# Optimization experiments

Measured on AMD Instinct MI355X. Metric: run time of the kernel, lower is better.

Reference implementation:

```python
import jax, jax.numpy as jnp
import numpy as np

N = 65536        # nodes
E = 1048576      # edges (avg degree 16)
IN, HID, OUT = 128, 64, 64


def setup_inputs() -> dict:
    key = jax.random.key(0)
    ks = jax.random.split(key, 6)
    x = jax.random.normal(ks[0], (N, IN), jnp.float32)
    edge_index = jax.random.randint(ks[1], (2, E), 0, N, jnp.int32)
    # Glorot-style init as in PyG GCNConv
    W1 = jax.random.normal(ks[2], (IN, HID), jnp.float32) * (1.0 / np.sqrt(IN))
    b1 = jnp.zeros((HID,), jnp.float32)
    W2 = jax.random.normal(ks[3], (HID, OUT), jnp.float32) * (1.0 / np.sqrt(HID))
    b2 = jnp.zeros((OUT,), jnp.float32)
    return {"x": x, "edge_index": edge_index, "W1": W1, "b1": b1, "W2": W2, "b2": b2}


def _gcn_conv(h, src, dst, dinv_sqrt, W, b):
    # PyG GCNConv: transform, then D^-1/2 A_hat D^-1/2 aggregation (A_hat has self-loops)
    h = h @ W                                   # [N, F_out]
    norm = dinv_sqrt[src] * dinv_sqrt[dst]      # [E+N]
    msg = h[src] * norm[:, None]                # gather + scale
    return jax.ops.segment_sum(msg, dst, num_segments=N) + b


def reference(x, edge_index, W1, b1, W2, b2):
    loops = jnp.arange(N, dtype=edge_index.dtype)
    src = jnp.concatenate([edge_index[0], loops])   # [E+N] with self-loops
    dst = jnp.concatenate([edge_index[1], loops])
    deg = jax.ops.segment_sum(jnp.ones_like(dst, x.dtype), dst, num_segments=N)
    dinv_sqrt = jax.lax.rsqrt(deg)                  # deg >= 1 thanks to self-loops
    h = jax.nn.relu(_gcn_conv(x, src, dst, dinv_sqrt, W1, b1))
    return _gcn_conv(h, src, dst, dinv_sqrt, W2, b2)
```

## Files before the change

### kernel.cpp

```cpp
#include <hip/hip_runtime.h>
#include <hip/hip_fp16.h>


#define N_NODES 65536
#define E_EDGES 1048576
#define F_IN    128
#define F_HID   64
#define CAPSH   6
#define GEMM1_BLOCKS (N_NODES / 64)
#define FILL_BLOCKS  ((E_EDGES / 4 / 256) * 8)

__device__ inline unsigned int pack_h2(float a, float b) {
    __half2 h = __floats2half2_rn(a, b);
    return *(unsigned int*)&h;
}

__device__ inline float4 h4_to_f4(uint2 q) {
    __half2 a = *(__half2*)&q.x;
    __half2 b = *(__half2*)&q.y;
    float2 fa = __half22float2(a), fb = __half22float2(b);
    return make_float4(fa.x, fa.y, fb.x, fb.y);
}

template <int F_K, bool SCALED>
__device__ inline void gemm_body(const float* __restrict__ h, const float* __restrict__ W,
                                 const int* __restrict__ cnt, __half* __restrict__ P,
                                 int bid) {
    int wave = __builtin_amdgcn_readfirstlane(threadIdx.x >> 6);
    int lane = threadIdx.x & 63;
    int v = bid * 64 + lane;
    const float4* hr = (const float4*)(h + (size_t)v * F_K);
    float4 acc[4];
#pragma unroll
    for (int j = 0; j < 4; ++j) acc[j] = make_float4(0.f, 0.f, 0.f, 0.f);
#pragma unroll 4
    for (int kb = 0; kb < F_K / 4; ++kb) {
        float4 hv = hr[kb];
#pragma unroll
        for (int r = 0; r < 4; ++r) {
            float hk = r == 0 ? hv.x : r == 1 ? hv.y : r == 2 ? hv.z : hv.w;
            const float4* Wr = (const float4*)(W + (size_t)(kb * 4 + r) * 64 + (wave << 4));
#pragma unroll
            for (int j = 0; j < 4; ++j) {
                float4 w = Wr[j];
                acc[j].x = fmaf(hk, w.x, acc[j].x);
                acc[j].y = fmaf(hk, w.y, acc[j].y);
                acc[j].z = fmaf(hk, w.z, acc[j].z);
                acc[j].w = fmaf(hk, w.w, acc[j].w);
            }
        }
    }
    float s = SCALED ? rsqrtf((float)cnt[v] + 1.0f) : 1.0f;
    __half* Pr = P + (size_t)v * 64 + (wave << 4);
    uint4 q0, q1;
    q0.x = pack_h2(acc[0].x * s, acc[0].y * s); q0.y = pack_h2(acc[0].z * s, acc[0].w * s);
    q0.z = pack_h2(acc[1].x * s, acc[1].y * s); q0.w = pack_h2(acc[1].z * s, acc[1].w * s);
    q1.x = pack_h2(acc[2].x * s, acc[2].y * s); q1.y = pack_h2(acc[2].z * s, acc[2].w * s);
    q1.z = pack_h2(acc[3].x * s, acc[3].y * s); q1.w = pack_h2(acc[3].z * s, acc[3].w * s);
    ((uint4*)Pr)[0] = q0;
    ((uint4*)Pr)[1] = q1;
}

__global__ __launch_bounds__(256) void k_fused(
        const float* __restrict__ x, const float* __restrict__ W1,
        __half* __restrict__ P,
        const int* __restrict__ src, const int* __restrict__ dst,
        int* __restrict__ cnt, unsigned short* __restrict__ csr) {
    if (blockIdx.x < GEMM1_BLOCKS) {
        gemm_body<F_IN, false>(x, W1, nullptr, P, blockIdx.x);
    } else {
        int fb    = blockIdx.x - GEMM1_BLOCKS;
        int g     = fb & 7;
        int chunk = fb >> 3;
        int i     = chunk * blockDim.x + threadIdx.x;
        int4 d = ((const int4*)dst)[i];
#pragma unroll
        for (int k = 0; k < 4; ++k) {
            int dv = k == 0 ? d.x : k == 1 ? d.y : k == 2 ? d.z : d.w;
            if ((dv >> 13) == g) {
                int pos = atomicAdd(&cnt[dv], 1);
                csr[(dv << CAPSH) + pos] = (unsigned short)src[4 * i + k];
            }
        }
    }
}

__global__ __launch_bounds__(256) void k_scale(
        __half* __restrict__ P, const int* __restrict__ cnt) {
    int t = blockIdx.x * blockDim.x + threadIdx.x;
    int v = t >> 2;
    float dv = rsqrtf((float)cnt[v] + 1.0f);
    uint4* p = (uint4*)(P + (size_t)v * 64) + (t & 3) * 2;
#pragma unroll
    for (int q = 0; q < 2; ++q) {
        uint4 u = p[q];
        unsigned int* w = (unsigned int*)&u;
#pragma unroll
        for (int j = 0; j < 4; ++j) {
            __half2 h = *(__half2*)&w[j];
            float2 f = __half22float2(h);
            w[j] = pack_h2(f.x * dv, f.y * dv);
        }
        p[q] = u;
    }
}

template <int F_K>
__global__ __launch_bounds__(256) void k_gemm(
        const float* __restrict__ h, const float* __restrict__ W,
        const int* __restrict__ cnt, __half* __restrict__ P) {
    gemm_body<F_K, true>(h, W, cnt, P, blockIdx.x);
}

template <bool RELU>
__global__ __launch_bounds__(256) void k_agg(
        const __half* __restrict__ P, const unsigned short* __restrict__ csr,
        const int* __restrict__ cnt, const float* __restrict__ b,
        float* __restrict__ out) {
    int lane = threadIdx.x & 63;
    int sub  = lane >> 4;
    int col4 = lane & 15;
    int wave  = (blockIdx.x * blockDim.x + threadIdx.x) >> 6;
    int nwave = (gridDim.x * blockDim.x) >> 6;
    float4 bias = ((const float4*)b)[col4];
    for (int v = wave; v < N_NODES; v += nwave) {
        int c    = cnt[v];
        float dv = rsqrtf((float)c + 1.0f);
        int sidx = csr[(v << CAPSH) + lane];
        float4 acc = make_float4(0.f, 0.f, 0.f, 0.f);
        if (sub == 0) {
            float4 p = h4_to_f4(((const uint2*)(P + (size_t)v * 64))[col4]);
            acc = p;
        }
        for (int i = 0; i < c; i += 16) {
#pragma unroll
            for (int u = 0; u < 4; ++u) {
                int e = i + sub + 4 * u;
                int s = __shfl(sidx, e);
                if (e < c) {
                    float4 p = h4_to_f4(((const uint2*)(P + (size_t)s * 64))[col4]);
                    acc.x += p.x; acc.y += p.y; acc.z += p.z; acc.w += p.w;
                }
            }
        }
        acc.x += __shfl_xor(acc.x, 16); acc.y += __shfl_xor(acc.y, 16);
        acc.z += __shfl_xor(acc.z, 16); acc.w += __shfl_xor(acc.w, 16);
        acc.x += __shfl_xor(acc.x, 32); acc.y += __shfl_xor(acc.y, 32);
        acc.z += __shfl_xor(acc.z, 32); acc.w += __shfl_xor(acc.w, 32);
        if (lane < 16) {
            float4 o;
            o.x = dv * acc.x + bias.x;
            o.y = dv * acc.y + bias.y;
            o.z = dv * acc.z + bias.z;
            o.w = dv * acc.w + bias.w;
            if (RELU) {
                o.x = o.x > 0.f ? o.x : 0.f;
                o.y = o.y > 0.f ? o.y : 0.f;
                o.z = o.z > 0.f ? o.z : 0.f;
                o.w = o.w > 0.f ? o.w : 0.f;
            }
            ((float4*)(out + (size_t)v * 64))[col4] = o;
        }
    }
}

extern "C" void kernel_launch(void* const* d_in, const int* in_sizes, int n_in,
                              void* d_out, int out_size, void* d_ws, size_t ws_size,
                              hipStream_t stream) {
    const float* x   = (const float*)d_in[0];
    const int*   ei  = (const int*)d_in[1];
    const float* W1  = (const float*)d_in[2];
    const float* b1  = (const float*)d_in[3];
    const float* W2  = (const float*)d_in[4];
    const float* b2  = (const float*)d_in[5];
    float*       out = (float*)d_out;

    const int* src = ei;
    const int* dst = ei + E_EDGES;

    int*            cnt = (int*)d_ws;
    unsigned short* csr = (unsigned short*)(cnt + N_NODES);
    __half*         P1  = (__half*)(csr + ((size_t)N_NODES << CAPSH));
    __half*         P2  = P1 + (size_t)N_NODES * 64;
    float*          H   = out;

    hipMemsetAsync(cnt, 0, N_NODES * sizeof(int), stream);

    k_fused<<<GEMM1_BLOCKS + FILL_BLOCKS, 256, 0, stream>>>(x, W1, P1, src, dst, cnt, csr);

    k_scale<<<N_NODES * 4 / 256, 256, 0, stream>>>(P1, cnt);

    k_agg<true><<<4096, 256, 0, stream>>>(P1, csr, cnt, b1, H);

    k_gemm<F_HID><<<N_NODES / 64, 256, 0, stream>>>(H, W2, cnt, P2);
    k_agg<false><<<4096, 256, 0, stream>>>(P2, csr, cnt, b2, out);
}
```

Before: 208.4 us.

## Interleave GEMM and CSR-fill blocks; prefetch next node and predicate gathers in aggregation

The fused kernel now interleaves GEMM1 blocks with CSR-fill blocks, 8 GEMM per 64 fill blocks. The aim is to mix compute-bound and atomic/memory-bound work across the GPU instead of running them in two phases. The aggregation kernel software-pipelines the per-node metadata by loading count, neighbour indices and the self row for the next node before processing the current one. It also issues gather loads unconditionally and masks them to zero, avoiding divergent branches. The masked loads read slot entries past the count, which may contain stale indices. These are still valid addresses because they are 16-bit indices into P, so they add extra memory traffic but stay safe.

```diff
diff --git a/kernel.cpp b/kernel.cpp
--- a/kernel.cpp
+++ b/kernel.cpp
@@ -7,8 +7,7 @@
 #define F_IN    128
 #define F_HID   64
 #define CAPSH   6
-#define GEMM1_BLOCKS (N_NODES / 64)
-#define FILL_BLOCKS  ((E_EDGES / 4 / 256) * 8)
+#define FUSED_BLOCKS 9216
 
 __device__ inline unsigned int pack_h2(float a, float b) {
     __half2 h = __floats2half2_rn(a, b);
@@ -66,12 +65,13 @@
         __half* __restrict__ P,
         const int* __restrict__ src, const int* __restrict__ dst,
         int* __restrict__ cnt, unsigned short* __restrict__ csr) {
-    if (blockIdx.x < GEMM1_BLOCKS) {
-        gemm_body<F_IN, false>(x, W1, nullptr, P, blockIdx.x);
+    int w = blockIdx.x / 72;
+    int r = blockIdx.x - w * 72;
+    if (r >= 64) {
+        gemm_body<F_IN, false>(x, W1, nullptr, cnt ? P : P, w * 8 + (r - 64));
     } else {
-        int fb    = blockIdx.x - GEMM1_BLOCKS;
-        int g     = fb & 7;
-        int chunk = fb >> 3;
+        int g     = r & 7;
+        int chunk = w * 8 + (r >> 3);
         int i     = chunk * blockDim.x + threadIdx.x;
         int4 d = ((const int4*)dst)[i];
 #pragma unroll
@@ -123,24 +123,37 @@
     int wave  = (blockIdx.x * blockDim.x + threadIdx.x) >> 6;
     int nwave = (gridDim.x * blockDim.x) >> 6;
     float4 bias = ((const float4*)b)[col4];
-    for (int v = wave; v < N_NODES; v += nwave) {
-        int c    = cnt[v];
+    int v = wave;
+    int c = 0, sidx = 0;
+    uint2 selfq = make_uint2(0u, 0u);
+    if (v < N_NODES) {
+        c     = cnt[v];
+        sidx  = csr[(v << CAPSH) + lane];
+        selfq = ((const uint2*)(P + (size_t)v * 64))[col4];
+    }
+    while (v < N_NODES) {
+        int vn = v + nwave;
+        int cn = 0, sidxn = 0;
+        uint2 selfqn = make_uint2(0u, 0u);
+        if (vn < N_NODES) {
+            cn     = cnt[vn];
+            sidxn  = csr[(vn << CAPSH) + lane];
+            selfqn = ((const uint2*)(P + (size_t)vn * 64))[col4];
+        }
         float dv = rsqrtf((float)c + 1.0f);
-        int sidx = csr[(v << CAPSH) + lane];
         float4 acc = make_float4(0.f, 0.f, 0.f, 0.f);
-        if (sub == 0) {
-            float4 p = h4_to_f4(((const uint2*)(P + (size_t)v * 64))[col4]);
-            acc = p;
-        }
+        if (sub == 0) acc = h4_to_f4(selfq);
         for (int i = 0; i < c; i += 16) {
 #pragma unroll
             for (int u = 0; u < 4; ++u) {
                 int e = i + sub + 4 * u;
                 int s = __shfl(sidx, e);
-                if (e < c) {
-                    float4 p = h4_to_f4(((const uint2*)(P + (size_t)s * 64))[col4]);
-                    acc.x += p.x; acc.y += p.y; acc.z += p.z; acc.w += p.w;
-                }
+                uint2 q = ((const uint2*)(P + (size_t)s * 64))[col4];
+                bool m = e < c;
+                q.x = m ? q.x : 0u;
+                q.y = m ? q.y : 0u;
+                float4 p = h4_to_f4(q);
+                acc.x += p.x; acc.y += p.y; acc.z += p.z; acc.w += p.w;
             }
         }
         acc.x += __shfl_xor(acc.x, 16); acc.y += __shfl_xor(acc.y, 16);
@@ -161,6 +174,7 @@
             }
             ((float4*)(out + (size_t)v * 64))[col4] = o;
         }
+        v = vn; c = cn; sidx = sidxn; selfq = selfqn;
     }
 }
 
@@ -186,7 +200,7 @@
 
     hipMemsetAsync(cnt, 0, N_NODES * sizeof(int), stream);
 
-    k_fused<<<GEMM1_BLOCKS + FILL_BLOCKS, 256, 0, stream>>>(x, W1, P1, src, dst, cnt, csr);
+    k_fused<<<FUSED_BLOCKS, 256, 0, stream>>>(x, W1, P1, src, dst, cnt, csr);
 
     k_scale<<<N_NODES * 4 / 256, 256, 0, stream>>>(P1, cnt);
 
```

Result: faster. 199.8 us (-4.1%).

## Interleave four nodes per wave in aggregation to raise memory-level parallelism

Applied to the files above, without the earlier changes.

Each wave in the aggregation kernel now processes four nodes at a time instead of looping over one node at a time. All index, count and self-row loads for the four nodes are issued up front, and gathers for all four are issued before any accumulation, so more memory requests are in flight per wave. The final store is spread so each 16-lane group writes a different node. This uses more registers, which may lower occupancy, and the wave loops up to the largest degree of its four nodes. It also hardcodes the grid of 4096 blocks to cover exactly N nodes.

```diff
diff --git a/kernel.cpp b/kernel.cpp
--- a/kernel.cpp
+++ b/kernel.cpp
@@ -112,6 +112,35 @@
     gemm_body<F_K, true>(h, W, cnt, P, blockIdx.x);
 }
 
+#define GATHER4(qq, sidx, cc)                                              \
+    if (i < cc) {                                                          \
+        _Pragma("unroll")                                                  \
+        for (int u = 0; u < 4; ++u) {                                      \
+            int e = i + sub + 4 * u;                                       \
+            int s = __shfl(sidx, e);                                       \
+            qq[u] = ((const uint2*)(P + (size_t)s * 64))[col4];            \
+        }                                                                  \
+    }
+
+#define ACC4(accv, qq, cc)                                                 \
+    if (i < cc) {                                                          \
+        _Pragma("unroll")                                                  \
+        for (int u = 0; u < 4; ++u) {                                      \
+            int e = i + sub + 4 * u;                                       \
+            bool m = e < cc;                                               \
+            uint2 q = qq[u];                                               \
+            q.x = m ? q.x : 0u; q.y = m ? q.y : 0u;                        \
+            float4 p = h4_to_f4(q);                                        \
+            accv.x += p.x; accv.y += p.y; accv.z += p.z; accv.w += p.w;    \
+        }                                                                  \
+    }
+
+#define FOLD(accv)                                                         \
+    accv.x += __shfl_xor(accv.x, 16); accv.y += __shfl_xor(accv.y, 16);    \
+    accv.z += __shfl_xor(accv.z, 16); accv.w += __shfl_xor(accv.w, 16);    \
+    accv.x += __shfl_xor(accv.x, 32); accv.y += __shfl_xor(accv.y, 32);    \
+    accv.z += __shfl_xor(accv.z, 32); accv.w += __shfl_xor(accv.w, 32);
+
 template <bool RELU>
 __global__ __launch_bounds__(256) void k_agg(
         const __half* __restrict__ P, const unsigned short* __restrict__ csr,
@@ -120,48 +149,47 @@
     int lane = threadIdx.x & 63;
     int sub  = lane >> 4;
     int col4 = lane & 15;
-    int wave  = (blockIdx.x * blockDim.x + threadIdx.x) >> 6;
-    int nwave = (gridDim.x * blockDim.x) >> 6;
+    int wid  = (blockIdx.x * blockDim.x + threadIdx.x) >> 6;
+    const int W = 16384;
+    int vA = wid, vB = wid + W, vC = wid + 2 * W, vD = wid + 3 * W;
+    int cA = cnt[vA], cB = cnt[vB], cC = cnt[vC], cD = cnt[vD];
+    int sA = csr[(vA << CAPSH) + lane], sB = csr[(vB << CAPSH) + lane];
+    int sC = csr[(vC << CAPSH) + lane], sD = csr[(vD << CAPSH) + lane];
+    uint2 qsA = ((const uint2*)(P + (size_t)vA * 64))[col4];
+    uint2 qsB = ((const uint2*)(P + (size_t)vB * 64))[col4];
+    uint2 qsC = ((const uint2*)(P + (size_t)vC * 64))[col4];
+    uint2 qsD = ((const uint2*)(P + (size_t)vD * 64))[col4];
+    float4 accA = make_float4(0.f, 0.f, 0.f, 0.f), accB = accA, accC = accA, accD = accA;
+    if (sub == 0) {
+        accA = h4_to_f4(qsA); accB = h4_to_f4(qsB);
+        accC = h4_to_f4(qsC); accD = h4_to_f4(qsD);
+    }
+    int cm = max(max(cA, cB), max(cC, cD));
+    for (int i = 0; i < cm; i += 16) {
+        uint2 qa[4], qb[4], qc[4], qd[4];
+        GATHER4(qa, sA, cA) GATHER4(qb, sB, cB)
+        GATHER4(qc, sC, cC) GATHER4(qd, sD, cD)
+        ACC4(accA, qa, cA) ACC4(accB, qb, cB)
+        ACC4(accC, qc, cC) ACC4(accD, qd, cD)
+    }
+    FOLD(accA) FOLD(accB) FOLD(accC) FOLD(accD)
+    int   vs = sub == 0 ? vA : sub == 1 ? vB : sub == 2 ? vC : vD;
+    int   cs = sub == 0 ? cA : sub == 1 ? cB : sub == 2 ? cC : cD;
+    float4 a = sub == 0 ? accA : sub == 1 ? accB : sub == 2 ? accC : accD;
+    float dv = rsqrtf((float)cs + 1.0f);
     float4 bias = ((const float4*)b)[col4];
-    for (int v = wave; v < N_NODES; v += nwave) {
-        int c    = cnt[v];
-        float dv = rsqrtf((float)c + 1.0f);
-        int sidx = csr[(v << CAPSH) + lane];
-        float4 acc = make_float4(0.f, 0.f, 0.f, 0.f);
-        if (sub == 0) {
-            float4 p = h4_to_f4(((const uint2*)(P + (size_t)v * 64))[col4]);
-            acc = p;
-        }
-        for (int i = 0; i < c; i += 16) {
-#pragma unroll
-            for (int u = 0; u < 4; ++u) {
-                int e = i + sub + 4 * u;
-                int s = __shfl(sidx, e);
-                if (e < c) {
-                    float4 p = h4_to_f4(((const uint2*)(P + (size_t)s * 64))[col4]);
-                    acc.x += p.x; acc.y += p.y; acc.z += p.z; acc.w += p.w;
-                }
-            }
-        }
-        acc.x += __shfl_xor(acc.x, 16); acc.y += __shfl_xor(acc.y, 16);
-        acc.z += __shfl_xor(acc.z, 16); acc.w += __shfl_xor(acc.w, 16);
-        acc.x += __shfl_xor(acc.x, 32); acc.y += __shfl_xor(acc.y, 32);
-        acc.z += __shfl_xor(acc.z, 32); acc.w += __shfl_xor(acc.w, 32);
-        if (lane < 16) {
-            float4 o;
-            o.x = dv * acc.x + bias.x;
-            o.y = dv * acc.y + bias.y;
-            o.z = dv * acc.z + bias.z;
-            o.w = dv * acc.w + bias.w;
-            if (RELU) {
-                o.x = o.x > 0.f ? o.x : 0.f;
-                o.y = o.y > 0.f ? o.y : 0.f;
-                o.z = o.z > 0.f ? o.z : 0.f;
-                o.w = o.w > 0.f ? o.w : 0.f;
-            }
-            ((float4*)(out + (size_t)v * 64))[col4] = o;
-        }
-    }
+    float4 o;
+    o.x = dv * a.x + bias.x;
+    o.y = dv * a.y + bias.y;
+    o.z = dv * a.z + bias.z;
+    o.w = dv * a.w + bias.w;
+    if (RELU) {
+        o.x = o.x > 0.f ? o.x : 0.f;
+        o.y = o.y > 0.f ? o.y : 0.f;
+        o.z = o.z > 0.f ? o.z : 0.f;
+        o.w = o.w > 0.f ? o.w : 0.f;
+    }
+    ((float4*)(out + (size_t)vs * 64))[col4] = o;
 }
 
 extern "C" void kernel_launch(void* const* d_in, const int* in_sizes, int n_in,
```

New measurement: 210.8 us. No clear change (+1.1%).
